# Kernel optimization log

Hardware: AMD Instinct MI355X
Metric: run time of the kernel (lower is better)

Reference implementation:

```python
import jax, jax.numpy as jnp
import numpy as np

D_MODEL = 1024
NUM_HEADS = 16
HEAD_DIM = D_MODEL // NUM_HEADS  # 64
MAX_REL = 512
NUM_EMB = 2 * MAX_REL + 1  # 1025
B, L = 2, 2048


def _glorot(key, shape):
    fan_in, fan_out = shape[0], shape[1]
    lim = jnp.sqrt(6.0 / (fan_in + fan_out))
    return jax.random.uniform(key, shape, jnp.float32, -lim, lim)


def setup_inputs() -> dict:
    key = jax.random.key(0)
    ks = jax.random.split(key, 9)
    return {
        "query": jax.random.normal(ks[0], (B, L, D_MODEL), jnp.float32),
        "key": jax.random.normal(ks[1], (B, L, D_MODEL), jnp.float32),
        "value": jax.random.normal(ks[2], (B, L, D_MODEL), jnp.float32),
        "wq": _glorot(ks[3], (D_MODEL, D_MODEL)), "bq": jnp.zeros((D_MODEL,), jnp.float32),
        "wk": _glorot(ks[4], (D_MODEL, D_MODEL)), "bk": jnp.zeros((D_MODEL,), jnp.float32),
        "wv": _glorot(ks[5], (D_MODEL, D_MODEL)), "bv": jnp.zeros((D_MODEL,), jnp.float32),
        "wo": _glorot(ks[6], (D_MODEL, D_MODEL)), "bo": jnp.zeros((D_MODEL,), jnp.float32),
        "rel_emb": _glorot(ks[7], (NUM_EMB, HEAD_DIM)),
    }


def _split_heads(x):
    b, l, _ = x.shape
    return x.reshape(b, l, NUM_HEADS, HEAD_DIM).transpose(0, 2, 1, 3)  # (b,h,l,d)


def reference(query, key, value, wq, bq, wk, bk, wv, bv, wo, bo, rel_emb):
    q = _split_heads(query @ wq + bq)  # (b,h,l,d)
    k = _split_heads(key @ wk + bk)
    v = _split_heads(value @ wv + bv)

    # content scores: (b,h,l,l)
    content = jnp.einsum('bhid,bhjd->bhij', q, k)

    # relative position scores. Original gathers E[clip(j-i)] -> (L,L,d) then
    # einsum('bhid,ijd->bhij'). Equivalent & cheaper: project q onto all
    # relative embeddings once, then gather along the relative-index axis.
    idx = jnp.arange(q.shape[2])
    final_mat = jnp.clip(idx[None, :] - idx[:, None], -MAX_REL, MAX_REL) + MAX_REL  # (L,L)
    q_rel = jnp.einsum('bhid,rd->bhir', q, rel_emb)  # (b,h,l,num_emb)
    position = jnp.take_along_axis(q_rel, final_mat[None, None, :, :], axis=-1)  # (b,h,l,l)

    scores = (content + position) / jnp.sqrt(jnp.float32(HEAD_DIM))
    weights = jax.nn.softmax(scores, axis=-1)  # no mask, dropout off (inference)
    out = jnp.einsum('bhij,bhjd->bhid', weights, v)  # (b,h,l,d)

    out = out.transpose(0, 2, 1, 3).reshape(query.shape[0], -1, D_MODEL)
    return out @ wo + bo
```

## Files before the change

### kernel.cpp

```cpp
#include <hip/hip_runtime.h>
#include <hip/hip_bf16.h>


typedef __attribute__((ext_vector_type(8))) short short8;
typedef __attribute__((ext_vector_type(4))) float floatx4;

#define L_SEQ 2048
#define D_MODEL 1024
#define NHEAD 16
#define DH 64
#define BH 32
#define MROWS 4096

__device__ inline float b2f(short s) {
    unsigned int u = ((unsigned int)(unsigned short)s) << 16;
    float f; __builtin_memcpy(&f, &u, 4); return f;
}
__device__ inline short f2b(float f) {
    unsigned int u; __builtin_memcpy(&u, &f, 4);
    u += 0x7fffu + ((u >> 16) & 1u);
    return (short)(u >> 16);
}
__device__ inline unsigned int pack2(float a, float b) {
    __hip_bfloat162 h = __float22bfloat162_rn(make_float2(a, b));
    unsigned int u; __builtin_memcpy(&u, &h, 4); return u;
}
__device__ inline void st2(short* p, unsigned int v) {
    __builtin_memcpy(p, &v, 4);
}
__device__ inline void async_cp16(short* lds, const short* g) {
    __builtin_amdgcn_global_load_lds(
        (const __attribute__((address_space(1))) unsigned int*)g,
        (__attribute__((address_space(3))) unsigned int*)lds, 16, 0, 0);
}

__global__ __launch_bounds__(256) void detect_dtype(
        const unsigned short* __restrict__ q, int* __restrict__ flag) {
    __shared__ int s[256];
    int tid = threadIdx.x, cnt = 0;
    for (int i = tid; i < 65536; i += 256)
        if ((q[i] & 0x7F80u) == 0x7F80u) cnt++;
    s[tid] = cnt; __syncthreads();
    for (int st = 128; st; st >>= 1) {
        if (tid < st) s[tid] += s[tid + st];
        __syncthreads();
    }
    if (tid == 0) *flag = (s[0] > 4) ? 1 : 0;
}

__global__ __launch_bounds__(256) void norm_small(
        const void* __restrict__ bq, const void* __restrict__ bk,
        const void* __restrict__ bv, const void* __restrict__ bo,
        const void* __restrict__ rel, float* __restrict__ bias4,
        short* __restrict__ relb, const int* __restrict__ flagp) {
    const int f32 = *flagp;
    int t = blockIdx.x * 256 + threadIdx.x;
    if (t < 4096) {
        const void* src = (t < 1024) ? bq : (t < 2048) ? bk : (t < 3072) ? bv : bo;
        int i = t & 1023;
        bias4[t] = f32 ? ((const float*)src)[i] : b2f(((const short*)src)[i]);
    } else if (t < 4096 + 65600) {
        int i = t - 4096;
        relb[i] = f32 ? f2b(((const float*)rel)[i]) : ((const short*)rel)[i];
    }
}

__global__ __launch_bounds__(256) void transpose4(
        const void* __restrict__ w0, const void* __restrict__ w1,
        const void* __restrict__ w2, const void* __restrict__ w3,
        short* __restrict__ dst, const int* __restrict__ flagp) {
    const int f32 = *flagp;
    __shared__ short tile[32][33];
    const void* src = (blockIdx.z == 0) ? w0 : (blockIdx.z == 1) ? w1
                    : (blockIdx.z == 2) ? w2 : w3;
    short* d = dst + (size_t)blockIdx.z * (D_MODEL * D_MODEL);
    int x = blockIdx.x * 32 + threadIdx.x;
    int y0 = blockIdx.y * 32;
    for (int yy = threadIdx.y; yy < 32; yy += 8) {
        size_t idx = (size_t)(y0 + yy) * D_MODEL + x;
        tile[yy][threadIdx.x] = f32 ? f2b(((const float*)src)[idx])
                                    : ((const short*)src)[idx];
    }
    __syncthreads();
    int x0 = blockIdx.x * 32;
    for (int yy = threadIdx.y; yy < 32; yy += 8)
        d[(size_t)(x0 + yy) * D_MODEL + y0 + threadIdx.x] = tile[threadIdx.x][yy];
}

__global__ __launch_bounds__(256) void convert3(
        const float* __restrict__ q, const float* __restrict__ k,
        const float* __restrict__ v, short* __restrict__ abf_q,
        short* __restrict__ abf_k, short* __restrict__ abf_v,
        const int* __restrict__ flagp) {
    if (!*flagp) return;
    const int z = blockIdx.y;
    const float* src = (z == 0) ? q : (z == 1) ? k : v;
    short* dst = (z == 0) ? abf_q : (z == 1) ? abf_k : abf_v;
    size_t i8 = ((size_t)blockIdx.x * 256 + threadIdx.x) * 8;
    float4 f0 = *(const float4*)(&src[i8]);
    float4 f1 = *(const float4*)(&src[i8 + 4]);
    uint4 s;
    s.x = pack2(f0.x, f0.y); s.y = pack2(f0.z, f0.w);
    s.z = pack2(f1.x, f1.y); s.w = pack2(f1.z, f1.w);
    *(uint4*)(&dst[i8]) = s;
}

__global__ __launch_bounds__(256) void proj_gemm(
        const void* __restrict__ Aq, const void* __restrict__ Ak,
        const void* __restrict__ Av, const short* __restrict__ Cq,
        const short* __restrict__ Ck, const short* __restrict__ Cv,
        const short* __restrict__ WT, const float* __restrict__ bias4,
        short* __restrict__ Qout, const int* __restrict__ flagp) {
    const int f32 = *flagp;
    const int z = blockIdx.z;
    const short* A_ = f32 ? ((z == 0) ? Cq : (z == 1) ? Ck : Cv)
                          : (const short*)((z == 0) ? Aq : (z == 1) ? Ak : Av);
    const short* BT = WT + (size_t)z * (D_MODEL * D_MODEL);
    const float* bias = bias4 + z * 1024;
    short* C = Qout + (size_t)z * ((size_t)MROWS * D_MODEL);
    const int K = D_MODEL;

    __shared__ short Alds[128 * 32];
    __shared__ short Blds[128 * 32];
    const int tid = threadIdx.x;
    const int w = tid >> 6, lane = tid & 63, cl = lane & 15, quad = lane >> 4;
    const int wr = w >> 1, wc = w & 1;
    const int m0 = blockIdx.y * 128, n0 = blockIdx.x * 128;
    const int grow = lane >> 2, gcol = (lane & 3) * 8;

    floatx4 acc[4][4];
    for (int i = 0; i < 4; i++)
        for (int j = 0; j < 4; j++)
            acc[i][j] = {0.f, 0.f, 0.f, 0.f};

    for (int k0 = 0; k0 < K; k0 += 32) {
        for (int s = 0; s < 2; s++) {
            int r = w * 32 + s * 16;
            async_cp16(&Blds[r * 32], &BT[(size_t)(n0 + r + grow) * K + k0 + gcol]);
            async_cp16(&Alds[r * 32], &A_[(size_t)(m0 + r + grow) * K + k0 + gcol]);
        }
        __syncthreads();

        short8 af[4], bfr[4];
        for (int mt = 0; mt < 4; mt++)
            af[mt] = *(const short8*)(&Alds[(wr * 64 + mt * 16 + cl) * 32 + quad * 8]);
        for (int nt = 0; nt < 4; nt++)
            bfr[nt] = *(const short8*)(&Blds[(wc * 64 + nt * 16 + cl) * 32 + quad * 8]);
        for (int mt = 0; mt < 4; mt++)
            for (int nt = 0; nt < 4; nt++)
                acc[mt][nt] = __builtin_amdgcn_mfma_f32_16x16x32_bf16(
                    af[mt], bfr[nt], acc[mt][nt], 0, 0, 0);
        __syncthreads();
    }

    for (int nt = 0; nt < 4; nt++) {
        int n = n0 + wc * 64 + nt * 16 + cl;
        float bv = bias[n];
        int h = n >> 6, d = n & 63;
        for (int mt = 0; mt < 4; mt++) {
            for (int r = 0; r < 4; r++) {
                int m = m0 + wr * 64 + mt * 16 + quad * 4 + r;
                float v = acc[mt][nt][r] + bv;
                int b = m >> 11, i = m & 2047;
                if (z < 2)
                    C[(((size_t)(b * NHEAD + h)) * L_SEQ + i) * DH + d] = f2b(v);
                else
                    C[(((size_t)(b * NHEAD + h)) * DH + d) * L_SEQ + i] = f2b(v);
            }
        }
    }
}

__global__ __launch_bounds__(256) void out_gemm(
        const short* __restrict__ A, const short* __restrict__ BT,
        const float* __restrict__ bias, void* __restrict__ C_,
        const int* __restrict__ flagp) {
    const int f32 = *flagp;
    const int K = D_MODEL, N = D_MODEL;
    __shared__ short Alds[128 * 32];
    __shared__ short Blds[64 * 32];
    const int tid = threadIdx.x;
    const int w = tid >> 6, lane = tid & 63, cl = lane & 15, quad = lane >> 4;
    const int wr = w >> 1, wc = w & 1;
    const int m0 = blockIdx.y * 128, n0 = blockIdx.x * 64;
    const int grow = lane >> 2, gcol = (lane & 3) * 8;

    floatx4 acc[4][2];
    for (int i = 0; i < 4; i++)
        for (int j = 0; j < 2; j++)
            acc[i][j] = {0.f, 0.f, 0.f, 0.f};

    for (int k0 = 0; k0 < K; k0 += 32) {
        for (int s = 0; s < 2; s++) {
            int r = w * 32 + s * 16;
            async_cp16(&Alds[r * 32], &A[(size_t)(m0 + r + grow) * K + k0 + gcol]);
        }
        {
            int r = w * 16;
            async_cp16(&Blds[r * 32], &BT[(size_t)(n0 + r + grow) * K + k0 + gcol]);
        }
        __syncthreads();

        short8 af[4], bfr[2];
        for (int mt = 0; mt < 4; mt++)
            af[mt] = *(const short8*)(&Alds[(wr * 64 + mt * 16 + cl) * 32 + quad * 8]);
        for (int nt = 0; nt < 2; nt++)
            bfr[nt] = *(const short8*)(&Blds[(wc * 32 + nt * 16 + cl) * 32 + quad * 8]);
        for (int mt = 0; mt < 4; mt++)
            for (int nt = 0; nt < 2; nt++)
                acc[mt][nt] = __builtin_amdgcn_mfma_f32_16x16x32_bf16(
                    af[mt], bfr[nt], acc[mt][nt], 0, 0, 0);
        __syncthreads();
    }

    for (int nt = 0; nt < 2; nt++) {
        int n = n0 + wc * 32 + nt * 16 + cl;
        float bv = bias[n];
        for (int mt = 0; mt < 4; mt++) {
            for (int r = 0; r < 4; r++) {
                int m = m0 + wr * 64 + mt * 16 + quad * 4 + r;
                float v = acc[mt][nt][r] + bv;
                if (f32) ((float*)C_)[(size_t)m * N + n] = v;
                else     ((short*)C_)[(size_t)m * N + n] = f2b(v);
            }
        }
    }
}

__global__ __launch_bounds__(256) void attn_kernel(
        const short* __restrict__ Q, const short* __restrict__ K,
        const short* __restrict__ VT, const short* __restrict__ rel,
        short* __restrict__ out) {
    const int tid = threadIdx.x;
    const int w = tid >> 6, lane = tid & 63, cl = lane & 15, quad = lane >> 4;
    const int bh = blockIdx.y, b = bh >> 4, h = bh & 15;
    const int I0 = blockIdx.x * 64;
    const int iw0 = I0 + w * 16;

    const short* Qp = Q + (size_t)bh * L_SEQ * DH;
    const short* Kp = K + (size_t)bh * L_SEQ * DH;
    const short* Vp = VT + (size_t)bh * DH * L_SEQ;

    __shared__ short Klds2[2][64 * 64];
    __shared__ short Vtlds2[2][64 * 64];
    __shared__ short PpLds[4][16 * 86];
    __shared__ short Plds[4][16 * 64];

    short* PpW = &PpLds[w][0];
    short* PW  = &Plds[w][0];

    short8 aq[2];
    for (int c = 0; c < 2; c++)
        aq[c] = *(const short8*)(&Qp[(size_t)(iw0 + cl) * DH + c * 32 + quad * 8]);

    const float SCALE2 = 0.125f * 1.44269504088896340736f;
    const float FMAX = 32.0f;

    float addlo, addhi;
    {
        floatx4 Dc = {0.f, 0.f, 0.f, 0.f};
        int eidx = (cl == 1) ? 1024 : 0;
        for (int c = 0; c < 2; c++) {
            short8 ae = *(const short8*)(&rel[(size_t)eidx * DH + c * 32 + quad * 8]);
            Dc = __builtin_amdgcn_mfma_f32_16x16x32_bf16(ae, aq[c], Dc, 0, 0, 0);
        }
        float pcl = __shfl(Dc[0], cl, 64);
        float pch = __shfl(Dc[1], cl, 64);
        addlo = fmaf(pcl, SCALE2, -FMAX);
        addhi = fmaf(pch, SCALE2, -FMAX);
    }

    floatx4 O[4];
    for (int dt = 0; dt < 4; dt++) O[dt] = {0.f, 0.f, 0.f, 0.f};
    float lsum = 0.f;

    const int lr = lane >> 3;
    const int lc8 = ((lane & 7) ^ lr) * 8;

    for (int s = 0; s < 2; s++) {
        int g = w * 2 + s;
        int r = g * 8 + lr;
        async_cp16(&Klds2[0][g * 512], &Kp[(size_t)r * DH + lc8]);
        async_cp16(&Vtlds2[0][g * 512], &Vp[(size_t)r * L_SEQ + lc8]);
    }
    int cur = 0;

    for (int j0 = 0; j0 < L_SEQ; j0 += 64) {
        __syncthreads();

        if (j0 + 64 < L_SEQ) {
            for (int s = 0; s < 2; s++) {
                int g = w * 2 + s;
                int r = g * 8 + lr;
                async_cp16(&Klds2[cur ^ 1][g * 512],
                           &Kp[(size_t)(j0 + 64 + r) * DH + lc8]);
                async_cp16(&Vtlds2[cur ^ 1][g * 512],
                           &Vp[(size_t)r * L_SEQ + (j0 + 64) + lc8]);
            }
        }
        const short* Kb = &Klds2[cur][0];
        const short* Vb = &Vtlds2[cur][0];

        const bool hi_clamp = (j0 - iw0 - 15) >= 512;
        const bool lo_clamp = (j0 + 63 - iw0) <= -512;
        const bool banded = !(hi_clamp || lo_clamp);
        const float addc = hi_clamp ? addhi : addlo;

        floatx4 St[4];
        for (int jt = 0; jt < 4; jt++) {
            St[jt] = {0.f, 0.f, 0.f, 0.f};
            int row = jt * 16 + cl;
            for (int c = 0; c < 2; c++) {
                int pos = ((4 * c + quad) ^ (cl & 7)) * 8;
                short8 bk = *(const short8*)(&Kb[row * 64 + pos]);
                St[jt] = __builtin_amdgcn_mfma_f32_16x16x32_bf16(bk, aq[c], St[jt], 0, 0, 0);
            }
        }

        if (banded) {
            floatx4 Pt[5];
            for (int pt = 0; pt < 5; pt++) Pt[pt] = {0.f, 0.f, 0.f, 0.f};
            const int base = j0 - iw0 - 15;
            for (int pt = 0; pt < 5; pt++) {
                int raw = pt * 16 + cl + base;
                int idx = (raw < -512 ? -512 : (raw > 512 ? 512 : raw)) + 512;
                const short* ep = rel + (size_t)idx * DH;
                for (int c = 0; c < 2; c++) {
                    short8 be = *(const short8*)(&ep[c * 32 + quad * 8]);
                    Pt[pt] = __builtin_amdgcn_mfma_f32_16x16x32_bf16(be, aq[c], Pt[pt], 0, 0, 0);
                }
            }
            for (int pt = 0; pt < 5; pt++) {
                int t = pt * 16 + quad * 4;
                st2(&PpW[cl * 86 + t],     pack2(Pt[pt][0], Pt[pt][1]));
                st2(&PpW[cl * 86 + t + 2], pack2(Pt[pt][2], Pt[pt][3]));
            }
            for (int jt = 0; jt < 4; jt++)
                for (int r = 0; r < 4; r++) {
                    int t = jt * 16 + quad * 4 + r - cl + 15;
                    float pos = b2f(PpW[cl * 86 + t]);
                    St[jt][r] = fmaf(St[jt][r], SCALE2, fmaf(pos, SCALE2, -FMAX));
                }
        } else {
            for (int jt = 0; jt < 4; jt++)
                for (int r = 0; r < 4; r++)
                    St[jt][r] = fmaf(St[jt][r], SCALE2, addc);
        }

        for (int jt = 0; jt < 4; jt++)
            for (int r = 0; r < 4; r++) {
                float p = __builtin_amdgcn_exp2f(St[jt][r]);
                St[jt][r] = p;
                lsum += p;
            }

        for (int jt = 0; jt < 4; jt++)
            for (int pr = 0; pr < 2; pr++) {
                int jl = jt * 16 + quad * 4 + pr * 2;
                int addr = cl * 64 + ((jl >> 3) ^ (cl & 7)) * 8 + (jl & 7);
                st2(&PW[addr], pack2(St[jt][2 * pr], St[jt][2 * pr + 1]));
            }

        for (int c = 0; c < 2; c++) {
            int ppos = ((4 * c + quad) ^ (cl & 7)) * 8;
            short8 bp = *(const short8*)(&PW[cl * 64 + ppos]);
            for (int dt = 0; dt < 4; dt++) {
                int row = dt * 16 + cl;
                int vpos = ((4 * c + quad) ^ (cl & 7)) * 8;
                short8 av = *(const short8*)(&Vb[row * 64 + vpos]);
                O[dt] = __builtin_amdgcn_mfma_f32_16x16x32_bf16(av, bp, O[dt], 0, 0, 0);
            }
        }
        cur ^= 1;
    }

    lsum += __shfl_xor(lsum, 16, 64);
    lsum += __shfl_xor(lsum, 32, 64);
    float inv = 1.0f / lsum;

    for (int dt = 0; dt < 4; dt++)
        for (int pr = 0; pr < 2; pr++) {
            int jl = dt * 16 + quad * 4 + pr * 2;
            int addr = cl * 64 + ((jl >> 3) ^ (cl & 7)) * 8 + (jl & 7);
            st2(&PW[addr], pack2(O[dt][2 * pr] * inv, O[dt][2 * pr + 1] * inv));
        }
    size_t obase = ((size_t)b * L_SEQ + iw0 + cl) * D_MODEL + h * DH;
    for (int s = 0; s < 2; s++) {
        int c2 = quad * 2 + s;
        short8 o = *(const short8*)(&PW[cl * 64 + (c2 ^ (cl & 7)) * 8]);
        *(short8*)(&out[obase + c2 * 8]) = o;
    }
}

extern "C" void kernel_launch(void* const* d_in, const int* in_sizes, int n_in,
                              void* d_out, int out_size, void* d_ws, size_t ws_size,
                              hipStream_t stream) {
    const void* query = d_in[0];
    const void* key   = d_in[1];
    const void* value = d_in[2];
    const void* wq = d_in[3];  const void* bq = d_in[4];
    const void* wk = d_in[5];  const void* bk = d_in[6];
    const void* wv = d_in[7];  const void* bv = d_in[8];
    const void* wo = d_in[9];  const void* bo = d_in[10];
    const void* rel = d_in[11];

    int* flag = (int*)d_ws;
    short* ws = (short*)d_ws + 16;
    const size_t WSZ = (size_t)D_MODEL * D_MODEL;
    const size_t TSZ = (size_t)MROWS * D_MODEL;
    short* WT   = ws;
    short* Qw   = ws + 4 * WSZ;
    short* Kw   = Qw + TSZ;
    short* Vtw  = Kw + TSZ;
    short* Attw = Vtw + TSZ;
    float* bias4 = (float*)(Attw + TSZ);
    short* relb  = (short*)(bias4 + 4096);

    short* Cq = (short*)d_out;
    short* Ck = (short*)d_out + TSZ;
    short* Cv = Attw;

    detect_dtype<<<1, 256, 0, stream>>>((const unsigned short*)query, flag);
    norm_small<<<273, 256, 0, stream>>>(bq, bk, bv, bo, rel, bias4, relb, flag);
    transpose4<<<dim3(32, 32, 4), dim3(32, 8), 0, stream>>>(wq, wk, wv, wo, WT, flag);

    convert3<<<dim3(2048, 3), 256, 0, stream>>>(
        (const float*)query, (const float*)key, (const float*)value,
        Cq, Ck, Cv, flag);

    proj_gemm<<<dim3(8, 32, 3), 256, 0, stream>>>(query, key, value,
                                                  Cq, Ck, Cv, WT, bias4,
                                                  Qw, flag);

    attn_kernel<<<dim3(L_SEQ / 64, BH), 256, 0, stream>>>(Qw, Kw, Vtw, relb, Attw);

    out_gemm<<<dim3(16, 32), 256, 0, stream>>>(Attw, WT + 3 * WSZ, bias4 + 3072,
                                               d_out, flag);
}
```

Baseline: 409.4 us.

## Process two 16-row query tiles per wave to reuse K/V LDS tiles

Each attention block now covers 128 query rows instead of 64, and each wave handles two 16-row query tiles against the same staged K and V^T tiles. The intent is to halve the global-to-LDS K/V traffic and the barrier count per unit of work. In exchange the grid shrinks to 512 blocks and per-thread register use grows with the doubled Q fragments and O accumulators, which may reduce occupancy and latency hiding on a 256-CU device.

```diff
diff --git a/kernel.cpp b/kernel.cpp
--- a/kernel.cpp
+++ b/kernel.cpp
@@ -234,8 +234,8 @@
     const int tid = threadIdx.x;
     const int w = tid >> 6, lane = tid & 63, cl = lane & 15, quad = lane >> 4;
     const int bh = blockIdx.y, b = bh >> 4, h = bh & 15;
-    const int I0 = blockIdx.x * 64;
-    const int iw0 = I0 + w * 16;
+    const int I0 = blockIdx.x * 128;
+    const int iw_base = I0 + w * 32;
 
     const short* Qp = Q + (size_t)bh * L_SEQ * DH;
     const short* Kp = K + (size_t)bh * L_SEQ * DH;
@@ -249,30 +249,36 @@
     short* PpW = &PpLds[w][0];
     short* PW  = &Plds[w][0];
 
-    short8 aq[2];
-    for (int c = 0; c < 2; c++)
-        aq[c] = *(const short8*)(&Qp[(size_t)(iw0 + cl) * DH + c * 32 + quad * 8]);
+    short8 aq[2][2];
+#pragma unroll
+    for (int it = 0; it < 2; it++)
+        for (int c = 0; c < 2; c++)
+            aq[it][c] = *(const short8*)(
+                &Qp[(size_t)(iw_base + it * 16 + cl) * DH + c * 32 + quad * 8]);
 
     const float SCALE2 = 0.125f * 1.44269504088896340736f;
     const float FMAX = 32.0f;
 
-    float addlo, addhi;
-    {
+    float addlo[2], addhi[2];
+#pragma unroll
+    for (int it = 0; it < 2; it++) {
         floatx4 Dc = {0.f, 0.f, 0.f, 0.f};
         int eidx = (cl == 1) ? 1024 : 0;
         for (int c = 0; c < 2; c++) {
             short8 ae = *(const short8*)(&rel[(size_t)eidx * DH + c * 32 + quad * 8]);
-            Dc = __builtin_amdgcn_mfma_f32_16x16x32_bf16(ae, aq[c], Dc, 0, 0, 0);
+            Dc = __builtin_amdgcn_mfma_f32_16x16x32_bf16(ae, aq[it][c], Dc, 0, 0, 0);
         }
         float pcl = __shfl(Dc[0], cl, 64);
         float pch = __shfl(Dc[1], cl, 64);
-        addlo = fmaf(pcl, SCALE2, -FMAX);
-        addhi = fmaf(pch, SCALE2, -FMAX);
-    }
-
-    floatx4 O[4];
-    for (int dt = 0; dt < 4; dt++) O[dt] = {0.f, 0.f, 0.f, 0.f};
-    float lsum = 0.f;
+        addlo[it] = fmaf(pcl, SCALE2, -FMAX);
+        addhi[it] = fmaf(pch, SCALE2, -FMAX);
+    }
+
+    floatx4 O[2][4];
+#pragma unroll
+    for (int it = 0; it < 2; it++)
+        for (int dt = 0; dt < 4; dt++) O[it][dt] = {0.f, 0.f, 0.f, 0.f};
+    float lsum0 = 0.f, lsum1 = 0.f;
 
     const int lr = lane >> 3;
     const int lc8 = ((lane & 7) ^ lr) * 8;
@@ -301,94 +307,107 @@
         const short* Kb = &Klds2[cur][0];
         const short* Vb = &Vtlds2[cur][0];
 
-        const bool hi_clamp = (j0 - iw0 - 15) >= 512;
-        const bool lo_clamp = (j0 + 63 - iw0) <= -512;
-        const bool banded = !(hi_clamp || lo_clamp);
-        const float addc = hi_clamp ? addhi : addlo;
-
-        floatx4 St[4];
-        for (int jt = 0; jt < 4; jt++) {
-            St[jt] = {0.f, 0.f, 0.f, 0.f};
-            int row = jt * 16 + cl;
-            for (int c = 0; c < 2; c++) {
-                int pos = ((4 * c + quad) ^ (cl & 7)) * 8;
-                short8 bk = *(const short8*)(&Kb[row * 64 + pos]);
-                St[jt] = __builtin_amdgcn_mfma_f32_16x16x32_bf16(bk, aq[c], St[jt], 0, 0, 0);
-            }
-        }
-
-        if (banded) {
-            floatx4 Pt[5];
-            for (int pt = 0; pt < 5; pt++) Pt[pt] = {0.f, 0.f, 0.f, 0.f};
-            const int base = j0 - iw0 - 15;
-            for (int pt = 0; pt < 5; pt++) {
-                int raw = pt * 16 + cl + base;
-                int idx = (raw < -512 ? -512 : (raw > 512 ? 512 : raw)) + 512;
-                const short* ep = rel + (size_t)idx * DH;
+#pragma unroll
+        for (int it = 0; it < 2; it++) {
+            const int iw = iw_base + it * 16;
+            const bool hi_clamp = (j0 - iw - 15) >= 512;
+            const bool lo_clamp = (j0 + 63 - iw) <= -512;
+            const bool banded = !(hi_clamp || lo_clamp);
+            const float addc = hi_clamp ? addhi[it] : addlo[it];
+
+            floatx4 St[4];
+            for (int jt = 0; jt < 4; jt++) {
+                St[jt] = {0.f, 0.f, 0.f, 0.f};
+                int row = jt * 16 + cl;
                 for (int c = 0; c < 2; c++) {
-                    short8 be = *(const short8*)(&ep[c * 32 + quad * 8]);
-                    Pt[pt] = __builtin_amdgcn_mfma_f32_16x16x32_bf16(be, aq[c], Pt[pt], 0, 0, 0);
-                }
-            }
-            for (int pt = 0; pt < 5; pt++) {
-                int t = pt * 16 + quad * 4;
-                st2(&PpW[cl * 86 + t],     pack2(Pt[pt][0], Pt[pt][1]));
-                st2(&PpW[cl * 86 + t + 2], pack2(Pt[pt][2], Pt[pt][3]));
-            }
+                    int pos = ((4 * c + quad) ^ (cl & 7)) * 8;
+                    short8 bk = *(const short8*)(&Kb[row * 64 + pos]);
+                    St[jt] = __builtin_amdgcn_mfma_f32_16x16x32_bf16(
+                        bk, aq[it][c], St[jt], 0, 0, 0);
+                }
+            }
+
+            if (banded) {
+                floatx4 Pt[5];
+                for (int pt = 0; pt < 5; pt++) Pt[pt] = {0.f, 0.f, 0.f, 0.f};
+                const int base = j0 - iw - 15;
+                for (int pt = 0; pt < 5; pt++) {
+                    int raw = pt * 16 + cl + base;
+                    int idx = (raw < -512 ? -512 : (raw > 512 ? 512 : raw)) + 512;
+                    const short* ep = rel + (size_t)idx * DH;
+                    for (int c = 0; c < 2; c++) {
+                        short8 be = *(const short8*)(&ep[c * 32 + quad * 8]);
+                        Pt[pt] = __builtin_amdgcn_mfma_f32_16x16x32_bf16(
+                            be, aq[it][c], Pt[pt], 0, 0, 0);
+                    }
+                }
+                for (int pt = 0; pt < 5; pt++) {
+                    int t = pt * 16 + quad * 4;
+                    st2(&PpW[cl * 86 + t],     pack2(Pt[pt][0], Pt[pt][1]));
+                    st2(&PpW[cl * 86 + t + 2], pack2(Pt[pt][2], Pt[pt][3]));
+                }
+                for (int jt = 0; jt < 4; jt++)
+                    for (int r = 0; r < 4; r++) {
+                        int t = jt * 16 + quad * 4 + r - cl + 15;
+                        float pos = b2f(PpW[cl * 86 + t]);
+                        St[jt][r] = fmaf(St[jt][r], SCALE2, fmaf(pos, SCALE2, -FMAX));
+                    }
+            } else {
+                for (int jt = 0; jt < 4; jt++)
+                    for (int r = 0; r < 4; r++)
+                        St[jt][r] = fmaf(St[jt][r], SCALE2, addc);
+            }
+
             for (int jt = 0; jt < 4; jt++)
                 for (int r = 0; r < 4; r++) {
-                    int t = jt * 16 + quad * 4 + r - cl + 15;
-                    float pos = b2f(PpW[cl * 86 + t]);
-                    St[jt][r] = fmaf(St[jt][r], SCALE2, fmaf(pos, SCALE2, -FMAX));
-                }
-        } else {
+                    float p = __builtin_amdgcn_exp2f(St[jt][r]);
+                    St[jt][r] = p;
+                    if (it == 0) lsum0 += p; else lsum1 += p;
+                }
+
             for (int jt = 0; jt < 4; jt++)
-                for (int r = 0; r < 4; r++)
-                    St[jt][r] = fmaf(St[jt][r], SCALE2, addc);
-        }
-
-        for (int jt = 0; jt < 4; jt++)
-            for (int r = 0; r < 4; r++) {
-                float p = __builtin_amdgcn_exp2f(St[jt][r]);
-                St[jt][r] = p;
-                lsum += p;
-            }
-
-        for (int jt = 0; jt < 4; jt++)
+                for (int pr = 0; pr < 2; pr++) {
+                    int jl = jt * 16 + quad * 4 + pr * 2;
+                    int addr = cl * 64 + ((jl >> 3) ^ (cl & 7)) * 8 + (jl & 7);
+                    st2(&PW[addr], pack2(St[jt][2 * pr], St[jt][2 * pr + 1]));
+                }
+
+            for (int c = 0; c < 2; c++) {
+                int ppos = ((4 * c + quad) ^ (cl & 7)) * 8;
+                short8 bp = *(const short8*)(&PW[cl * 64 + ppos]);
+                for (int dt = 0; dt < 4; dt++) {
+                    int row = dt * 16 + cl;
+                    int vpos = ((4 * c + quad) ^ (cl & 7)) * 8;
+                    short8 av = *(const short8*)(&Vb[row * 64 + vpos]);
+                    O[it][dt] = __builtin_amdgcn_mfma_f32_16x16x32_bf16(
+                        av, bp, O[it][dt], 0, 0, 0);
+                }
+            }
+        }
+        cur ^= 1;
+    }
+
+#pragma unroll
+    for (int it = 0; it < 2; it++) {
+        float lsum = (it == 0) ? lsum0 : lsum1;
+        lsum += __shfl_xor(lsum, 16, 64);
+        lsum += __shfl_xor(lsum, 32, 64);
+        float inv = 1.0f / lsum;
+
+        for (int dt = 0; dt < 4; dt++)
             for (int pr = 0; pr < 2; pr++) {
-                int jl = jt * 16 + quad * 4 + pr * 2;
+                int jl = dt * 16 + quad * 4 + pr * 2;
                 int addr = cl * 64 + ((jl >> 3) ^ (cl & 7)) * 8 + (jl & 7);
-                st2(&PW[addr], pack2(St[jt][2 * pr], St[jt][2 * pr + 1]));
-            }
-
-        for (int c = 0; c < 2; c++) {
-            int ppos = ((4 * c + quad) ^ (cl & 7)) * 8;
-            short8 bp = *(const short8*)(&PW[cl * 64 + ppos]);
-            for (int dt = 0; dt < 4; dt++) {
-                int row = dt * 16 + cl;
-                int vpos = ((4 * c + quad) ^ (cl & 7)) * 8;
-                short8 av = *(const short8*)(&Vb[row * 64 + vpos]);
-                O[dt] = __builtin_amdgcn_mfma_f32_16x16x32_bf16(av, bp, O[dt], 0, 0, 0);
-            }
-        }
-        cur ^= 1;
-    }
-
-    lsum += __shfl_xor(lsum, 16, 64);
-    lsum += __shfl_xor(lsum, 32, 64);
-    float inv = 1.0f / lsum;
-
-    for (int dt = 0; dt < 4; dt++)
-        for (int pr = 0; pr < 2; pr++) {
-            int jl = dt * 16 + quad * 4 + pr * 2;
-            int addr = cl * 64 + ((jl >> 3) ^ (cl & 7)) * 8 + (jl & 7);
-            st2(&PW[addr], pack2(O[dt][2 * pr] * inv, O[dt][2 * pr + 1] * inv));
-        }
-    size_t obase = ((size_t)b * L_SEQ + iw0 + cl) * D_MODEL + h * DH;
-    for (int s = 0; s < 2; s++) {
-        int c2 = quad * 2 + s;
-        short8 o = *(const short8*)(&PW[cl * 64 + (c2 ^ (cl & 7)) * 8]);
-        *(short8*)(&out[obase + c2 * 8]) = o;
+                st2(&PW[addr], pack2(O[it][dt][2 * pr] * inv,
+                                     O[it][dt][2 * pr + 1] * inv));
+            }
+        size_t obase = ((size_t)b * L_SEQ + iw_base + it * 16 + cl) * D_MODEL
+                     + h * DH;
+        for (int s = 0; s < 2; s++) {
+            int c2 = quad * 2 + s;
+            short8 o = *(const short8*)(&PW[cl * 64 + (c2 ^ (cl & 7)) * 8]);
+            *(short8*)(&out[obase + c2 * 8]) = o;
+        }
     }
 }
 
@@ -432,7 +451,7 @@
                                                   Cq, Ck, Cv, WT, bias4,
                                                   Qw, flag);
 
-    attn_kernel<<<dim3(L_SEQ / 64, BH), 256, 0, stream>>>(Qw, Kw, Vtw, relb, Attw);
+    attn_kernel<<<dim3(L_SEQ / 128, BH), 256, 0, stream>>>(Qw, Kw, Vtw, relb, Attw);
 
     out_gemm<<<dim3(16, 32), 256, 0, stream>>>(Attw, WT + 3 * WSZ, bias4 + 3072,
                                                d_out, flag);
```

Measured after the change: 415.4 us. Within noise of the previous version (+1.5%).
